# Kernel tuning notes

Measured on AMD Instinct MI355X. Metric: run time of the kernel, lower is better.

Reference implementation:

```python
import jax, jax.numpy as jnp
import numpy as np

B, S, N = 1, 128, 256
C_IN, C_H, C_OUT = 256, 32, 128
EPS = 1e-5


def setup_inputs() -> dict:
    key = jax.random.key(0)
    k_m, k_wa, k_wb, k_wo = jax.random.split(key, 4)
    m = jax.random.normal(k_m, (B, S, N, C_IN), dtype=jnp.float32)
    mask = jnp.ones((B, S, N), dtype=jnp.float32)
    gamma = jnp.ones((C_IN,), dtype=jnp.float32)
    beta = jnp.zeros((C_IN,), dtype=jnp.float32)
    # nn.Linear weights are (out, in)
    Wa = jax.random.normal(k_wa, (C_H, C_IN), dtype=jnp.float32) / np.sqrt(C_IN).astype(np.float32)
    Wb = jax.random.normal(k_wb, (C_H, C_IN), dtype=jnp.float32) / np.sqrt(C_IN).astype(np.float32)
    # proj_o is final_init (zeros) in the source; use small random weights so the
    # baseline output is non-trivial for correctness checking.
    Wo = jax.random.normal(k_wo, (C_OUT, C_H * C_H), dtype=jnp.float32) / np.sqrt(C_H * C_H).astype(np.float32)
    bo = jnp.zeros((C_OUT,), dtype=jnp.float32)
    return {"m": m, "mask": mask, "gamma": gamma, "beta": beta,
            "Wa": Wa, "Wb": Wb, "Wo": Wo, "bo": bo}


def reference(m, mask, gamma, beta, Wa, Wb, Wo, bo):
    # LayerNorm over c_in
    mu = jnp.mean(m, axis=-1, keepdims=True)
    var = jnp.mean((m - mu) ** 2, axis=-1, keepdims=True)
    mn = (m - mu) * jax.lax.rsqrt(var + EPS) * gamma + beta  # (B,S,N,c_in)

    mk = mask[..., None]  # (B,S,N,1)
    a = jnp.einsum('bsni,hi->bsnh', mn, Wa) * mk  # (B,S,N,c_h)
    b = jnp.einsum('bsni,hi->bsnh', mn, Wb) * mk  # (B,S,N,c_h)

    # pairwise mask count over S, clamped to >= 1
    num_mask = jnp.clip(jnp.einsum('bsi,bsj->bij', mask, mask), 1.0, None)  # (B,N,N)

    # outer-product mean over the sequence dim
    z = jnp.einsum('bsic,bsjd->bijcd', a, b)  # (B,N,N,c_h,c_h)
    z = z.reshape(z.shape[0], z.shape[1], z.shape[2], C_H * C_H)
    z = z / num_mask[..., None]

    return jnp.einsum('bijk,ok->bijo', z, Wo) + bo  # (B,N,N,c_out)
```

## Files before the change

kernel.cpp:

```cpp
#include <hip/hip_runtime.h>
#include <hip/hip_bf16.h>

#define S_DIM 128
#define N_DIM 256
#define CIN   256
#define CH    32
#define COUT  128

typedef __attribute__((ext_vector_type(8))) short bf16x8;
typedef __attribute__((ext_vector_type(4))) float f32x4;
typedef __attribute__((ext_vector_type(16))) float f32x16;

__device__ __forceinline__ unsigned short f2bf(float f) {
  union { float f; unsigned int u; } v; v.f = f;
  unsigned int u = v.u;
  return (unsigned short)((u + 0x7FFFu + ((u >> 16) & 1u)) >> 16);
}

__device__ __forceinline__ unsigned int pk2(float x, float y) {
  float2 f2; f2.x = x; f2.y = y;
  __hip_bfloat162 h = __float22bfloat162_rn(f2);
  union { __hip_bfloat162 h; unsigned int u; } c; c.h = h;
  return c.u;
}

__global__ __launch_bounds__(256) void lnp_prep_kernel(
    const float* __restrict__ m, const float* __restrict__ mask,
    const float* __restrict__ gamma, const float* __restrict__ beta,
    const float* __restrict__ Wa, const float* __restrict__ Wb,
    const float* __restrict__ Wo,
    float* __restrict__ rnm, unsigned short* __restrict__ wo3,
    unsigned short* __restrict__ a_t, unsigned short* __restrict__ b_t) {
  const int b = blockIdx.x, t = threadIdx.x;
  if (b < 1024) {
    __shared__ __align__(16) unsigned short mn[32][264];
    __shared__ __align__(16) unsigned short wabs[64 * 256];
    const int i = b & 255, s0 = (b >> 8) * 32;
    const int w = t >> 6, l = t & 63, lq = l >> 4, lr = l & 15;

    #pragma unroll
    for (int it = 0; it < 8; it++) {
      const int gi = it * 256 + t;
      const int r = gi >> 5, g = gi & 31;
      const float* src = (r < 32) ? (Wa + r * 256 + g * 8)
                                  : (Wb + (r - 32) * 256 + g * 8);
      const int gp = (g & 16) | ((g ^ (r & 15)) & 15);
      const float4 v0 = *(const float4*)(src);
      const float4 v1 = *(const float4*)(src + 4);
      uint4 qv;
      qv.x = pk2(v0.x, v0.y); qv.y = pk2(v0.z, v0.w);
      qv.z = pk2(v1.x, v1.y); qv.w = pk2(v1.z, v1.w);
      *(uint4*)(&wabs[r * 256 + gp * 8]) = qv;
    }

    const float4 g4 = *(const float4*)(gamma + l * 4);
    const float4 b4 = *(const float4*)(beta + l * 4);

    float4 mv[8];
    float mkv[8];
    #pragma unroll
    for (int rr = 0; rr < 8; rr++) {
      const int s = s0 + w * 8 + rr;
      mv[rr] = *(const float4*)(m + ((size_t)(s * N_DIM + i)) * CIN + l * 4);
      mkv[rr] = mask[s * N_DIM + i];
    }

    #pragma unroll
    for (int rr = 0; rr < 8; rr++) {
      const int r = w * 8 + rr;
      const float4 v = mv[rr];
      float sum = v.x + v.y + v.z + v.w;
      float sq  = v.x * v.x + v.y * v.y + v.z * v.z + v.w * v.w;
      #pragma unroll
      for (int off = 32; off > 0; off >>= 1) {
        sum += __shfl_down(sum, off);
        sq  += __shfl_down(sq, off);
      }
      sum = __shfl(sum, 0); sq = __shfl(sq, 0);
      const float mu = sum * (1.0f / CIN);
      const float var = fmaxf(sq * (1.0f / CIN) - mu * mu, 0.0f);
      const float rs = rsqrtf(var + 1e-5f);
      const float mk = mkv[rr];
      uint2 p2;
      p2.x = pk2(((v.x - mu) * rs * g4.x + b4.x) * mk,
                 ((v.y - mu) * rs * g4.y + b4.y) * mk);
      p2.y = pk2(((v.z - mu) * rs * g4.z + b4.z) * mk,
                 ((v.w - mu) * rs * g4.w + b4.w) * mk);
      *(uint2*)(&mn[r][l * 4]) = p2;
    }
    __syncthreads();

    const int wm = w & 1;
    const int n2 = w >> 1;
    f32x4 acc0 = {0.f, 0.f, 0.f, 0.f}, acc1 = {0.f, 0.f, 0.f, 0.f};
    #pragma unroll
    for (int ks = 0; ks < 8; ks++) {
      const int k0 = ks * 32 + lq * 8;
      const int g = ks * 4 + lq;
      const int gp = (g & 16) | ((g ^ lr) & 15);
      const bf16x8 af = *(const bf16x8*)(&mn[wm * 16 + lr][k0]);
      const bf16x8 bf0 = *(const bf16x8*)(&wabs[(n2 * 32 + lr) * 256 + gp * 8]);
      const bf16x8 bf1 = *(const bf16x8*)(&wabs[(n2 * 32 + 16 + lr) * 256 + gp * 8]);
      acc0 = __builtin_amdgcn_mfma_f32_16x16x32_bf16(af, bf0, acc0, 0, 0, 0);
      acc1 = __builtin_amdgcn_mfma_f32_16x16x32_bf16(af, bf1, acc1, 0, 0, 0);
    }

    unsigned short* dst = (n2 == 0) ? a_t : b_t;
    const int scol = s0 + wm * 16 + lq * 4;
    uint2 q0, q1;
    q0.x = pk2(acc0[0], acc0[1]); q0.y = pk2(acc0[2], acc0[3]);
    q1.x = pk2(acc1[0], acc1[1]); q1.y = pk2(acc1[2], acc1[3]);
    *(uint2*)(dst + ((size_t)(i * CH + lr)) * S_DIM + scol) = q0;
    *(uint2*)(dst + ((size_t)(i * CH + 16 + lr)) * S_DIM + scol) = q1;
  } else if (b < 1152) {
    const int r = b - 1024;
    #pragma unroll
    for (int q = 0; q < 4; q++) {
      const int f = r * 1024 + q * 256 + t;
      const int e = f & 7, l = (f >> 3) & 63;
      const int step = (f >> 9) & 63, og = f >> 15;
      const int kp = step * 16 + (l >> 5) * 8 + e;
      const int c = kp & 31, d = kp >> 5;
      const int o = og * 32 + (l & 31);
      wo3[f] = f2bf(Wo[o * 1024 + c * 32 + d]);
    }
  } else {
    const int i = b - 1152;
    float acc = 0.f;
    #pragma unroll 8
    for (int s = 0; s < S_DIM; s++)
      acc += mask[s * N_DIM + i] * mask[s * N_DIM + t];
    acc = fmaxf(acc, 1.0f);
    rnm[i * N_DIM + t] = 1.0f / acc;
  }
}

__global__ __launch_bounds__(512, 4) void fused_kernel(
    const unsigned short* __restrict__ a_t, const unsigned short* __restrict__ b_t,
    const unsigned short* __restrict__ wo3, const float* __restrict__ rnm,
    const float* __restrict__ bo, float* __restrict__ out) {
  extern __shared__ __align__(16) unsigned short smem[];
  unsigned short* sA = smem;
  unsigned short* sB = smem + 16384;
  unsigned short* sZ = smem;

  const int t = threadIdx.x, w = t >> 6, l = t & 63;
  const int lq = l >> 4, lr = l & 15;
  const int bx = blockIdx.x, by = blockIdx.y;

  const unsigned short* srcA = a_t + (size_t)bx * 32768;
  const unsigned short* srcB = b_t + (size_t)by * 16384;

  const int og = w & 3;
  const int pA = l & 31;
  const unsigned short* wop = wo3 + ((size_t)(og * 64) * 64 + l) * 8;

  const int wy = (w >> 1) * 64, wx = (w & 1) * 64;
  f32x4 acc[4][4];
  #pragma unroll
  for (int a = 0; a < 4; a++)
    #pragma unroll
    for (int c = 0; c < 4; c++) acc[a][c] = (f32x4){0.f, 0.f, 0.f, 0.f};

  #pragma unroll 1
  for (int h = 0; h < 2; h++) {
    if (h) __syncthreads();
    #pragma unroll
    for (int it = 0; it < 4; it++) {
      const int idx = it * 512 + t;
      const int r = idx >> 3, g = idx & 7;
      const bf16x8 v = *(const bf16x8*)(srcA + r * 128 + h * 64 + g * 8);
      *(bf16x8*)(&sA[r * 64 + ((g ^ (r & 7)) << 3)]) = v;
    }
    #pragma unroll
    for (int it = 0; it < 2; it++) {
      const int idx = it * 512 + t;
      const int r = idx >> 3, g = idx & 7;
      const bf16x8 v = *(const bf16x8*)(srcB + r * 128 + h * 64 + g * 8);
      *(bf16x8*)(&sB[r * 64 + ((g ^ (r & 7)) << 3)]) = v;
    }
    __syncthreads();

    #pragma unroll
    for (int ks2 = 0; ks2 < 2; ks2++) {
      const int gi = ks2 * 4 + lq;
      bf16x8 afr[4], bfr[4];
      #pragma unroll
      for (int a = 0; a < 4; a++) {
        const int ra = wy + a * 16 + lr;
        afr[a] = *(const bf16x8*)(&sA[ra * 64 + ((gi ^ (ra & 7)) << 3)]);
        const int rb = wx + a * 16 + lr;
        bfr[a] = *(const bf16x8*)(&sB[rb * 64 + ((gi ^ (rb & 7)) << 3)]);
      }
      #pragma unroll
      for (int a = 0; a < 4; a++)
        #pragma unroll
        for (int c = 0; c < 4; c++)
          acc[a][c] = __builtin_amdgcn_mfma_f32_16x16x32_bf16(afr[a], bfr[c], acc[a][c], 0, 0, 0);
    }
  }

  bf16x8 wfb0[4], wfb1[4];
  if (w < 4) {
    #pragma unroll
    for (int q = 0; q < 4; q++)
      wfb0[q] = *(const bf16x8*)(wop + (size_t)q * 512);
  }

  __syncthreads();

  #pragma unroll
  for (int a = 0; a < 4; a++) {
    #pragma unroll
    for (int c = 0; c < 4; c++) {
      const int zrb = wy + a * 16 + lq * 4;
      const int zc  = wx + c * 16 + lr;
      const int pr = (zrb >> 5) * 4 + (zc >> 5);
      const int off = (zc & 31) * 32 + (zrb & 31);
      const int g = off >> 3;
      const int gp = (g & ~7) | ((g ^ (g >> 3) ^ pr) & 7);
      uint2 q;
      q.x = pk2(acc[a][c][0], acc[a][c][1]);
      q.y = pk2(acc[a][c][2], acc[a][c][3]);
      *(uint2*)(&sZ[pr * 1024 + gp * 8 + (off & 7)]) = q;
    }
  }
  __syncthreads();

  if (w >= 4) return;

  #pragma unroll
  for (int q = 0; q < 4; q++)
    wfb1[q] = *(const bf16x8*)(wop + (size_t)(4 + q) * 512);

  const int o = og * 32 + (l & 31);
  const float bov = bo[o];
  float scv[16];
  #pragma unroll
  for (int r = 0; r < 16; r++) {
    const int row = (r & 3) + 8 * (r >> 2) + 4 * (l >> 5);
    const int ii = bx * 8 + (row >> 2), jj = by * 4 + (row & 3);
    scv[r] = rnm[ii * N_DIM + jj];
  }

  f32x16 acc2;
  #pragma unroll
  for (int r = 0; r < 16; r++) acc2[r] = 0.f;

  #pragma unroll
  for (int jb = 0; jb < 16; jb++) {
    #pragma unroll
    for (int q = 0; q < 4; q++) {
      const int s = jb * 4 + q;
      const int g = s * 2 + (l >> 5);
      const int gA = (g & ~7) | ((g ^ (g >> 3) ^ pA) & 7);
      const bf16x8 zf = *(const bf16x8*)(&sZ[pA * 1024 + gA * 8]);
      const bf16x8 wf = (jb & 1) ? wfb1[q] : wfb0[q];
      acc2 = __builtin_amdgcn_mfma_f32_32x32x16_bf16(zf, wf, acc2, 0, 0, 0);
    }
    if (jb < 14) {
      #pragma unroll
      for (int q = 0; q < 4; q++) {
        const bf16x8 v = *(const bf16x8*)(wop + (size_t)((jb + 2) * 4 + q) * 512);
        if (jb & 1) wfb1[q] = v; else wfb0[q] = v;
      }
    }
  }

  #pragma unroll
  for (int r = 0; r < 16; r++) {
    const int row = (r & 3) + 8 * (r >> 2) + 4 * (l >> 5);
    const int ii = bx * 8 + (row >> 2), jj = by * 4 + (row & 3);
    out[((size_t)(ii * N_DIM + jj)) * COUT + o] = acc2[r] * scv[r] + bov;
  }
}

extern "C" void kernel_launch(void* const* d_in, const int* in_sizes, int n_in,
                              void* d_out, int out_size, void* d_ws, size_t ws_size,
                              hipStream_t stream) {
  const float* m     = (const float*)d_in[0];
  const float* mask  = (const float*)d_in[1];
  const float* gamma = (const float*)d_in[2];
  const float* beta  = (const float*)d_in[3];
  const float* Wa    = (const float*)d_in[4];
  const float* Wb    = (const float*)d_in[5];
  const float* Wo    = (const float*)d_in[6];
  const float* bo    = (const float*)d_in[7];
  float* out = (float*)d_out;

  char* ws = (char*)d_ws;
  float*          rnm = (float*)(ws);
  unsigned short* wo3 = (unsigned short*)(ws + 262144);
  unsigned short* a_t = (unsigned short*)(ws + 524288);
  unsigned short* b_t = (unsigned short*)(ws + 2621440);

  hipFuncSetAttribute((const void*)fused_kernel,
                      hipFuncAttributeMaxDynamicSharedMemorySize, 65536);

  lnp_prep_kernel<<<1408, 256, 0, stream>>>(m, mask, gamma, beta, Wa, Wb, Wo,
                                            rnm, wo3, a_t, b_t);
  fused_kernel<<<dim3(32, 64), 512, 65536, stream>>>(a_t, b_t, wo3, rnm, bo, out);
}
```

Baseline: 139.9 us.

## Split output projection across all eight waves using 16x16 MFMA tiles

The second-stage projection from the pair tile to the output channels now runs on all 8 waves instead of 4. Each wave owns 16 output channels and computes two 16x16 tiles with 16x16x32 MFMAs, where before 4 waves each did a 32x32 tile. The Wo repacking in the prep kernel changes to the matching 16-channel fragment layout. This doubles the waves doing work in the tail phase but adds more LDS reads of the Z tile, since each wave now reads both row halves.

```diff
diff --git a/kernel.cpp b/kernel.cpp
--- a/kernel.cpp
+++ b/kernel.cpp
@@ -118,10 +118,10 @@
     for (int q = 0; q < 4; q++) {
       const int f = r * 1024 + q * 256 + t;
       const int e = f & 7, l = (f >> 3) & 63;
-      const int step = (f >> 9) & 63, og = f >> 15;
-      const int kp = step * 16 + (l >> 5) * 8 + e;
+      const int s = (f >> 9) & 31, o16 = f >> 14;
+      const int kp = s * 32 + ((l >> 4) & 3) * 8 + e;
       const int c = kp & 31, d = kp >> 5;
-      const int o = og * 32 + (l & 31);
+      const int o = o16 * 16 + (l & 15);
       wo3[f] = f2bf(Wo[o * 1024 + c * 32 + d]);
     }
   } else {
@@ -151,9 +151,8 @@
   const unsigned short* srcA = a_t + (size_t)bx * 32768;
   const unsigned short* srcB = b_t + (size_t)by * 16384;
 
-  const int og = w & 3;
-  const int pA = l & 31;
-  const unsigned short* wop = wo3 + ((size_t)(og * 64) * 64 + l) * 8;
+  const int m16 = l & 15, kq16 = l >> 4;
+  const unsigned short* wop = wo3 + ((size_t)(w * 32) * 64 + l) * 8;
 
   const int wy = (w >> 1) * 64, wx = (w & 1) * 64;
   f32x4 acc[4][4];
@@ -201,11 +200,9 @@
   }
 
   bf16x8 wfb0[4], wfb1[4];
-  if (w < 4) {
-    #pragma unroll
-    for (int q = 0; q < 4; q++)
-      wfb0[q] = *(const bf16x8*)(wop + (size_t)q * 512);
-  }
+  #pragma unroll
+  for (int q = 0; q < 4; q++)
+    wfb0[q] = *(const bf16x8*)(wop + (size_t)q * 512);
 
   __syncthreads();
 
@@ -227,38 +224,38 @@
   }
   __syncthreads();
 
-  if (w >= 4) return;
-
   #pragma unroll
   for (int q = 0; q < 4; q++)
     wfb1[q] = *(const bf16x8*)(wop + (size_t)(4 + q) * 512);
 
-  const int o = og * 32 + (l & 31);
+  const int o = w * 16 + m16;
   const float bov = bo[o];
-  float scv[16];
-  #pragma unroll
-  for (int r = 0; r < 16; r++) {
-    const int row = (r & 3) + 8 * (r >> 2) + 4 * (l >> 5);
-    const int ii = bx * 8 + (row >> 2), jj = by * 4 + (row & 3);
-    scv[r] = rnm[ii * N_DIM + jj];
-  }
-
-  f32x16 acc2;
-  #pragma unroll
-  for (int r = 0; r < 16; r++) acc2[r] = 0.f;
-
-  #pragma unroll
-  for (int jb = 0; jb < 16; jb++) {
+  float sca[4], scb[4];
+  #pragma unroll
+  for (int r = 0; r < 4; r++) {
+    const int pa = kq16 * 4 + r;
+    sca[r] = rnm[(bx * 8 + (pa >> 2)) * N_DIM + by * 4 + (pa & 3)];
+    const int pb = 16 + pa;
+    scb[r] = rnm[(bx * 8 + (pb >> 2)) * N_DIM + by * 4 + (pb & 3)];
+  }
+
+  f32x4 acc2a = {0.f, 0.f, 0.f, 0.f}, acc2b = {0.f, 0.f, 0.f, 0.f};
+
+  #pragma unroll
+  for (int jb = 0; jb < 8; jb++) {
     #pragma unroll
     for (int q = 0; q < 4; q++) {
       const int s = jb * 4 + q;
-      const int g = s * 2 + (l >> 5);
-      const int gA = (g & ~7) | ((g ^ (g >> 3) ^ pA) & 7);
-      const bf16x8 zf = *(const bf16x8*)(&sZ[pA * 1024 + gA * 8]);
+      const int g = s * 4 + kq16;
+      const int gA = (g & ~7) | ((g ^ (g >> 3) ^ m16) & 7);
+      const int gB = (g & ~7) | ((g ^ (g >> 3) ^ (16 + m16)) & 7);
+      const bf16x8 zfA = *(const bf16x8*)(&sZ[m16 * 1024 + gA * 8]);
+      const bf16x8 zfB = *(const bf16x8*)(&sZ[(16 + m16) * 1024 + gB * 8]);
       const bf16x8 wf = (jb & 1) ? wfb1[q] : wfb0[q];
-      acc2 = __builtin_amdgcn_mfma_f32_32x32x16_bf16(zf, wf, acc2, 0, 0, 0);
-    }
-    if (jb < 14) {
+      acc2a = __builtin_amdgcn_mfma_f32_16x16x32_bf16(zfA, wf, acc2a, 0, 0, 0);
+      acc2b = __builtin_amdgcn_mfma_f32_16x16x32_bf16(zfB, wf, acc2b, 0, 0, 0);
+    }
+    if (jb < 6) {
       #pragma unroll
       for (int q = 0; q < 4; q++) {
         const bf16x8 v = *(const bf16x8*)(wop + (size_t)((jb + 2) * 4 + q) * 512);
@@ -268,10 +265,13 @@
   }
 
   #pragma unroll
-  for (int r = 0; r < 16; r++) {
-    const int row = (r & 3) + 8 * (r >> 2) + 4 * (l >> 5);
-    const int ii = bx * 8 + (row >> 2), jj = by * 4 + (row & 3);
-    out[((size_t)(ii * N_DIM + jj)) * COUT + o] = acc2[r] * scv[r] + bov;
+  for (int r = 0; r < 4; r++) {
+    const int pa = kq16 * 4 + r;
+    out[((size_t)((bx * 8 + (pa >> 2)) * N_DIM + by * 4 + (pa & 3))) * COUT + o] =
+        acc2a[r] * sca[r] + bov;
+    const int pb = 16 + pa;
+    out[((size_t)((bx * 8 + (pb >> 2)) * N_DIM + by * 4 + (pb & 3))) * COUT + o] =
+        acc2b[r] * scb[r] + bov;
   }
 }
 
```

Result: no change. 141.8 us (+1.4%).
